# Optimization experiments

Hardware: AMD Instinct MI355X
Metric: run time of the kernel (lower is better)

Reference implementation:

```python
import jax, jax.numpy as jnp
import numpy as np

EPS = 1e-10

def _iou(a, b):
    """IoU for boxes in (cx, cy, w, h) format; a, b: (..., 4)."""
    a_min = a[..., :2] - a[..., 2:] * 0.5
    a_max = a[..., :2] + a[..., 2:] * 0.5
    b_min = b[..., :2] - b[..., 2:] * 0.5
    b_max = b[..., :2] + b[..., 2:] * 0.5
    inter_wh = jnp.clip(jnp.minimum(a_max, b_max) - jnp.maximum(a_min, b_min), 0.0)
    inter = inter_wh[..., 0] * inter_wh[..., 1]
    area_a = a[..., 2] * a[..., 3]
    area_b = b[..., 2] * b[..., 3]
    return inter / (area_a + area_b - inter + EPS)

def setup_inputs() -> dict:
    key = jax.random.key(0)
    k1, k2, k3 = jax.random.split(key, 3)
    BATCH, S, C = 16384, 7, 30
    # uniform in (0.01, 1) so sqrt() of w,h channels is finite/differentiable
    preds = jax.random.uniform(k1, (BATCH, S, S, C), jnp.float32, 0.01, 1.0)
    labels = jax.random.uniform(k2, (BATCH, S, S, C), jnp.float32, 0.01, 1.0)
    obj = jax.random.bernoulli(k3, 0.15, (BATCH, S, S)).astype(jnp.float32)
    labels = labels.at[..., 4].set(obj)  # code branches on labels[...,4] == 1
    return {"preds": preds, "labels": labels}

def reference(preds, labels):
    batch = preds.shape[0]
    obj = labels[..., 4] == 1.0  # (B, S, S)
    # faithful quirk: label bbox x-coord is read transposed (labels[i, y, x, 0])
    lb0 = jnp.swapaxes(labels[..., 0], 1, 2)
    lbox = jnp.stack([lb0, labels[..., 1], labels[..., 2], labels[..., 3]], axis=-1)
    iou1 = _iou(preds[..., 0:4], lbox)
    iou2 = _iou(preds[..., 5:9], lbox)
    choose1 = iou1 > iou2
    # branch where box 1 is responsible
    b1 = (5.0 * jnp.sum((preds[..., 0:2] - labels[..., 0:2]) ** 2, -1)
          + jnp.sum((jnp.sqrt(preds[..., 2:4]) - jnp.sqrt(labels[..., 2:4])) ** 2, -1)
          + (iou1 - preds[..., 4]) ** 2
          + 0.5 * preds[..., 9] ** 2)
    # branch where box 2 is responsible (targets read from labels[...,5:9] as in source)
    b2 = (5.0 * jnp.sum((preds[..., 5:7] - labels[..., 5:7]) ** 2, -1)
          + jnp.sum((jnp.sqrt(preds[..., 7:9]) - jnp.sqrt(labels[..., 7:9])) ** 2, -1)
          + (iou2 - preds[..., 9]) ** 2
          + 0.5 * preds[..., 4] ** 2)
    cls = jnp.sum((labels[..., 10:] - preds[..., 10:]) ** 2, -1)
    obj_loss = jnp.where(choose1, b1, b2) + cls
    noobj_loss = 0.5 * (preds[..., 4] ** 2 + preds[..., 9] ** 2)
    total = jnp.sum(jnp.where(obj, obj_loss, noobj_loss))
    return total / batch
```

## Files before the change

kernel.cpp:

```cpp
#include <hip/hip_runtime.h>


#define BATCH 16384
#define S 7
#define C 30
#define NCELLS (BATCH * S * S)
#define BLOCK 256
#define NBLK (NCELLS / BLOCK)

__device__ __forceinline__ float sq(float v) { return v * v; }

__device__ __forceinline__ float iou_box(float acx, float acy, float aw, float ah,
                                         float bcx, float bcy, float bw, float bh) {
    float ax0 = acx - aw * 0.5f, ax1 = acx + aw * 0.5f;
    float ay0 = acy - ah * 0.5f, ay1 = acy + ah * 0.5f;
    float bx0 = bcx - bw * 0.5f, bx1 = bcx + bw * 0.5f;
    float by0 = bcy - bh * 0.5f, by1 = bcy + bh * 0.5f;
    float iw = fmaxf(fminf(ax1, bx1) - fmaxf(ax0, bx0), 0.0f);
    float ih = fmaxf(fminf(ay1, by1) - fmaxf(ay0, by0), 0.0f);
    float inter = iw * ih;
    float denom = aw * ah + bw * bh - inter + 1e-10f;
    return inter / denom;
}

__global__ __launch_bounds__(BLOCK, 2) void yolo_partial_kernel(
        const float* __restrict__ preds,
        const float* __restrict__ labels,
        float* __restrict__ partials) {
    const int tid  = threadIdx.x;
    const int cell = blockIdx.x * BLOCK + tid;

    int b    = cell / (S * S);
    int rem  = cell - b * (S * S);
    int y    = rem / S;
    int x    = rem - y * S;
    int pc   = b * (S * S) + x * S + y;

    const float2* pG = reinterpret_cast<const float2*>(preds  + (size_t)cell * C);
    const float2* lG = reinterpret_cast<const float2*>(labels + (size_t)cell * C);

    float2 tp[15], tl[15];
    #pragma unroll
    for (int i = 0; i < 15; ++i) tp[i] = pG[i];
    #pragma unroll
    for (int i = 0; i < 15; ++i) tl[i] = lG[i];
    float lb0 = labels[(size_t)pc * C];

    float pv[C], lv[C];
    #pragma unroll
    for (int i = 0; i < 15; ++i) {
        pv[2 * i] = tp[i].x; pv[2 * i + 1] = tp[i].y;
        lv[2 * i] = tl[i].x; lv[2 * i + 1] = tl[i].y;
    }

    float iou1 = iou_box(pv[0], pv[1], pv[2], pv[3], lb0, lv[1], lv[2], lv[3]);
    float iou2 = iou_box(pv[5], pv[6], pv[7], pv[8], lb0, lv[1], lv[2], lv[3]);

    float b1 = 5.0f * (sq(pv[0] - lv[0]) + sq(pv[1] - lv[1]))
             + sq(sqrtf(pv[2]) - sqrtf(lv[2])) + sq(sqrtf(pv[3]) - sqrtf(lv[3]))
             + sq(iou1 - pv[4])
             + 0.5f * pv[9] * pv[9];

    float b2 = 5.0f * (sq(pv[5] - lv[5]) + sq(pv[6] - lv[6]))
             + sq(sqrtf(pv[7]) - sqrtf(lv[7])) + sq(sqrtf(pv[8]) - sqrtf(lv[8]))
             + sq(iou2 - pv[9])
             + 0.5f * pv[4] * pv[4];

    float cls = 0.0f;
    #pragma unroll
    for (int c = 10; c < C; ++c) cls += sq(lv[c] - pv[c]);

    float obj_loss   = ((iou1 > iou2) ? b1 : b2) + cls;
    float noobj_loss = 0.5f * (pv[4] * pv[4] + pv[9] * pv[9]);
    float loss = (lv[4] == 1.0f) ? obj_loss : noobj_loss;

    #pragma unroll
    for (int off = 32; off > 0; off >>= 1)
        loss += __shfl_down(loss, off, 64);

    __shared__ float wsum[BLOCK / 64];
    int lane = tid & 63;
    int wv   = tid >> 6;
    if (lane == 0) wsum[wv] = loss;
    __syncthreads();
    if (tid == 0) {
        partials[blockIdx.x] = wsum[0] + wsum[1] + wsum[2] + wsum[3];
    }
}

__global__ __launch_bounds__(BLOCK) void yolo_reduce_kernel(
        const float* __restrict__ partials,
        float* __restrict__ out) {
    const int tid = threadIdx.x;
    float s = 0.0f;
    for (int i = tid; i < NBLK; i += BLOCK) s += partials[i];

    #pragma unroll
    for (int off = 32; off > 0; off >>= 1)
        s += __shfl_down(s, off, 64);

    __shared__ float wsum[BLOCK / 64];
    int lane = tid & 63;
    int wv   = tid >> 6;
    if (lane == 0) wsum[wv] = s;
    __syncthreads();
    if (tid == 0) {
        out[0] = (wsum[0] + wsum[1] + wsum[2] + wsum[3]) * (1.0f / (float)BATCH);
    }
}

extern "C" void kernel_launch(void* const* d_in, const int* in_sizes, int n_in,
                              void* d_out, int out_size, void* d_ws, size_t ws_size,
                              hipStream_t stream) {
    const float* preds  = (const float*)d_in[0];
    const float* labels = (const float*)d_in[1];
    float* out = (float*)d_out;
    float* partials = (float*)d_ws;

    yolo_partial_kernel<<<NBLK, BLOCK, 0, stream>>>(preds, labels, partials);
    yolo_reduce_kernel<<<1, BLOCK, 0, stream>>>(partials, out);
}
```

Before: 218.3 us.

## Use persistent grid with register double-buffered prefetch across four cells per thread

Shrinks the grid to 784 blocks, each thread handling four cells strided by the grid size. The next cell's preds, labels and partner label are loaded into registers while the current cell's loss is computed, so memory latency overlaps with math. Launch bounds rise to 3 blocks per CU. This roughly doubles register demand from the prefetch buffers, which may cause spills or lower occupancy.

```diff
diff --git a/kernel.cpp b/kernel.cpp
--- a/kernel.cpp
+++ b/kernel.cpp
@@ -6,7 +6,9 @@
 #define C 30
 #define NCELLS (BATCH * S * S)
 #define BLOCK 256
-#define NBLK (NCELLS / BLOCK)
+#define GRID 784
+#define ITERS 4
+#define STRIDE (GRID * BLOCK)
 
 __device__ __forceinline__ float sq(float v) { return v * v; }
 
@@ -23,29 +25,15 @@
     return inter / denom;
 }
 
-__global__ __launch_bounds__(BLOCK, 2) void yolo_partial_kernel(
-        const float* __restrict__ preds,
-        const float* __restrict__ labels,
-        float* __restrict__ partials) {
-    const int tid  = threadIdx.x;
-    const int cell = blockIdx.x * BLOCK + tid;
+__device__ __forceinline__ int partner_cell(int cell) {
+    int b   = cell / (S * S);
+    int rem = cell - b * (S * S);
+    int y   = rem / S;
+    int x   = rem - y * S;
+    return b * (S * S) + x * S + y;
+}
 
-    int b    = cell / (S * S);
-    int rem  = cell - b * (S * S);
-    int y    = rem / S;
-    int x    = rem - y * S;
-    int pc   = b * (S * S) + x * S + y;
-
-    const float2* pG = reinterpret_cast<const float2*>(preds  + (size_t)cell * C);
-    const float2* lG = reinterpret_cast<const float2*>(labels + (size_t)cell * C);
-
-    float2 tp[15], tl[15];
-    #pragma unroll
-    for (int i = 0; i < 15; ++i) tp[i] = pG[i];
-    #pragma unroll
-    for (int i = 0; i < 15; ++i) tl[i] = lG[i];
-    float lb0 = labels[(size_t)pc * C];
-
+__device__ __forceinline__ float cell_loss(const float2* tp, const float2* tl, float lb0) {
     float pv[C], lv[C];
     #pragma unroll
     for (int i = 0; i < 15; ++i) {
@@ -72,16 +60,61 @@
 
     float obj_loss   = ((iou1 > iou2) ? b1 : b2) + cls;
     float noobj_loss = 0.5f * (pv[4] * pv[4] + pv[9] * pv[9]);
-    float loss = (lv[4] == 1.0f) ? obj_loss : noobj_loss;
+    return (lv[4] == 1.0f) ? obj_loss : noobj_loss;
+}
+
+__global__ __launch_bounds__(BLOCK, 3) void yolo_partial_kernel(
+        const float* __restrict__ preds,
+        const float* __restrict__ labels,
+        float* __restrict__ partials) {
+    const int tid   = threadIdx.x;
+    const int cell0 = blockIdx.x * BLOCK + tid;
+
+    float2 tp[15], tl[15];
+    float  lb0;
+    {
+        const float2* pG = reinterpret_cast<const float2*>(preds  + (size_t)cell0 * C);
+        const float2* lG = reinterpret_cast<const float2*>(labels + (size_t)cell0 * C);
+        #pragma unroll
+        for (int i = 0; i < 15; ++i) tp[i] = pG[i];
+        #pragma unroll
+        for (int i = 0; i < 15; ++i) tl[i] = lG[i];
+        lb0 = labels[(size_t)partner_cell(cell0) * C];
+    }
+
+    float acc = 0.0f;
+    #pragma unroll
+    for (int it = 0; it < ITERS; ++it) {
+        float2 np[15], nl[15];
+        float  nlb0 = 0.0f;
+        if (it + 1 < ITERS) {
+            int nc = cell0 + (it + 1) * STRIDE;
+            const float2* pG = reinterpret_cast<const float2*>(preds  + (size_t)nc * C);
+            const float2* lG = reinterpret_cast<const float2*>(labels + (size_t)nc * C);
+            #pragma unroll
+            for (int i = 0; i < 15; ++i) np[i] = pG[i];
+            #pragma unroll
+            for (int i = 0; i < 15; ++i) nl[i] = lG[i];
+            nlb0 = labels[(size_t)partner_cell(nc) * C];
+        }
+
+        acc += cell_loss(tp, tl, lb0);
+
+        if (it + 1 < ITERS) {
+            #pragma unroll
+            for (int i = 0; i < 15; ++i) { tp[i] = np[i]; tl[i] = nl[i]; }
+            lb0 = nlb0;
+        }
+    }
 
     #pragma unroll
     for (int off = 32; off > 0; off >>= 1)
-        loss += __shfl_down(loss, off, 64);
+        acc += __shfl_down(acc, off, 64);
 
     __shared__ float wsum[BLOCK / 64];
     int lane = tid & 63;
     int wv   = tid >> 6;
-    if (lane == 0) wsum[wv] = loss;
+    if (lane == 0) wsum[wv] = acc;
     __syncthreads();
     if (tid == 0) {
         partials[blockIdx.x] = wsum[0] + wsum[1] + wsum[2] + wsum[3];
@@ -93,7 +126,7 @@
         float* __restrict__ out) {
     const int tid = threadIdx.x;
     float s = 0.0f;
-    for (int i = tid; i < NBLK; i += BLOCK) s += partials[i];
+    for (int i = tid; i < GRID; i += BLOCK) s += partials[i];
 
     #pragma unroll
     for (int off = 32; off > 0; off >>= 1)
@@ -117,6 +150,6 @@
     float* out = (float*)d_out;
     float* partials = (float*)d_ws;
 
-    yolo_partial_kernel<<<NBLK, BLOCK, 0, stream>>>(preds, labels, partials);
+    yolo_partial_kernel<<<GRID, BLOCK, 0, stream>>>(preds, labels, partials);
     yolo_reduce_kernel<<<1, BLOCK, 0, stream>>>(partials, out);
 }
```

After: 242.7 us. 11.1% more time.
